# Performance work log

Measured on AMD Instinct MI355X. Metric: run time of the kernel, lower is better.

The kernel has to match this reference:

```python
import jax, jax.numpy as jnp
import numpy as np

NUM_HEAD = 8   # in_channels // 64 for in_channels=512
DIM = 8        # per-head dim (== num_head in this module)
H_CH = NUM_HEAD * DIM  # 64
SCALE = DIM ** (-0.5)


def _conv(x, w, b, padding):
    # x: [N,C,H,W], w: [O,I,kh,kw]
    out = jax.lax.conv_general_dilated(
        x, w, window_strides=(1, 1), padding=padding,
        dimension_numbers=("NCHW", "OIHW", "NCHW"))
    return out + b[None, :, None, None]


def setup_inputs() -> dict:
    key = jax.random.key(0)
    ks = jax.random.split(key, 4)
    N, C, H, W = 4, 512, 48, 48
    x = jax.random.normal(ks[0], (N, C, H, W), dtype=jnp.float32)
    qkv_w = jax.random.normal(ks[1], (3 * H_CH, C, 1, 1), dtype=jnp.float32) * 0.05
    qkv_b = jnp.zeros((3 * H_CH,), dtype=jnp.float32)
    pos_w = jax.random.normal(ks[2], (H_CH, H_CH, 3, 3), dtype=jnp.float32) * 0.05
    pos_b = jnp.zeros((H_CH,), dtype=jnp.float32)
    res_w = jax.random.normal(ks[3], (C, H_CH, 1, 1), dtype=jnp.float32) * 0.05
    res_b = jnp.zeros((C,), dtype=jnp.float32)
    return {"x": x, "qkv_w": qkv_w, "qkv_b": qkv_b,
            "pos_w": pos_w, "pos_b": pos_b,
            "res_w": res_w, "res_b": res_b}


def reference(x, qkv_w, qkv_b, pos_w, pos_b, res_w, res_b):
    N, C, H, W = x.shape
    L = H * W
    # 1x1 conv QKV projection -> [N, 3h, H, W]
    qkv = _conv(x, qkv_w, qkv_b, "VALID")
    # [N, num_head, 3*dim, L]
    qkv = qkv.reshape(N, NUM_HEAD, 3 * DIM, L)
    q, k, v = qkv[:, :, :DIM], qkv[:, :, DIM:2 * DIM], qkv[:, :, 2 * DIM:]
    # attn = q^T @ k * scale : [N, nh, L, L], softmax over keys (last dim)
    attn = jnp.einsum("nhdq,nhdk->nhqk", q, k) * SCALE
    attn = jax.nn.softmax(attn, axis=-1)
    # out = v @ attn^T : [N, nh, dim, L]
    out = jnp.einsum("nhdk,nhqk->nhdq", v, attn)
    out = out.reshape(N, H_CH, H, W)
    # positional branch: 3x3 conv on v
    pos = _conv(v.reshape(N, H_CH, H, W), pos_w, pos_b, "SAME")
    out = out + pos
    # resume 1x1 conv -> [N, out_channels, H, W]
    return _conv(out, res_w, res_b, "VALID")
```

## Files before the change

kernel.cpp:

```cpp
#include <hip/hip_runtime.h>

#define L_ATT 2304
#define QSCALE_LOG2E 0.5100695712f

using bh8 = __attribute__((ext_vector_type(8))) short;
using f4  = __attribute__((ext_vector_type(4))) float;

#if __has_builtin(__builtin_amdgcn_exp2f)
#define EXP2(x) __builtin_amdgcn_exp2f(x)
#else
#define EXP2(x) exp2f(x)
#endif

__device__ inline short f2b(float f) {
    union { float f; unsigned u; } c; c.f = f;
    unsigned r = (c.u + 0x7FFFu + ((c.u >> 16) & 1u)) >> 16;
    return (short)r;
}
__device__ inline float b2f(short s) {
    union { unsigned u; float f; } c;
    c.u = ((unsigned)(unsigned short)s) << 16;
    return c.f;
}
__device__ inline int packhi(float lo, float hi) {
    return (int)__builtin_amdgcn_perm(__float_as_uint(hi), __float_as_uint(lo), 0x07060302u);
}

__global__ __launch_bounds__(256) void prep_kernel(
    const float* __restrict__ x, const float* __restrict__ qkv_w,
    const float* __restrict__ res_w, const float* __restrict__ pos_w,
    short* __restrict__ xt, short* __restrict__ wqb,
    short* __restrict__ reswb, short* __restrict__ wqp)
{
    __shared__ float s[64][68];
    const int g = blockIdx.x;
    if (g < 272) {
        int j = g * 256 + threadIdx.x;
        if (j < 24576) {
            float4 v = ((const float4*)qkv_w)[j];
            short4 o = { f2b(v.x), f2b(v.y), f2b(v.z), f2b(v.w) };
            *(short4*)(wqb + (size_t)j * 4) = o;
        } else if (j < 32768) {
            int idx = j - 24576;
            float4 v = ((const float4*)res_w)[idx];
            short4 o = { f2b(v.x), f2b(v.y), f2b(v.z), f2b(v.w) };
            *(short4*)(reswb + (size_t)idx * 4) = o;
        } else {
            int e = j - 32768;
            wqp[e] = f2b(pos_w[(size_t)(e & 4095) * 9 + (e >> 12)]);
        }
        return;
    }
    const int gg = g - 272;
    const int l0 = (gg % 36) * 64, k0 = ((gg / 36) & 7) * 64, n = gg / 288;
    const int tr = threadIdx.x >> 4, tc4 = (threadIdx.x & 15) * 4;
    const float* xp = x + ((size_t)n * 512 + k0) * L_ATT + l0;
#pragma unroll
    for (int r = 0; r < 4; ++r)
        *(float4*)&s[tr + r * 16][tc4] =
            *(const float4*)(xp + (size_t)(tr + r * 16) * L_ATT + tc4);
    __syncthreads();
    short* op = xt + ((size_t)n * L_ATT + l0) * 512 + k0;
#pragma unroll
    for (int r = 0; r < 4; ++r) {
        int l = tr + r * 16;
        short4 o = { f2b(s[tc4 + 0][l]), f2b(s[tc4 + 1][l]),
                     f2b(s[tc4 + 2][l]), f2b(s[tc4 + 3][l]) };
        *(short4*)(op + (size_t)l * 512 + tc4) = o;
    }
}

__global__ __launch_bounds__(256) void qkv_kernel(
    const short* __restrict__ xt, const short* __restrict__ wqb,
    const float* __restrict__ qkv_b, short* __restrict__ qt8,
    short* __restrict__ kt8, short* __restrict__ vt, short* __restrict__ vle)
{
    const int g = blockIdx.x;
    const int xcd = g & 7, rr = g >> 3;
    const int y = rr % 3, grp = rr / 3;
    const int code = grp * 8 + xcd;
    const int l0 = (code % 72) * 32, oc0 = y * 64, n = code / 72;

    const int lane = threadIdx.x & 63, wave = threadIdx.x >> 6;
    const int col = lane & 15, quad = lane >> 4;
    const int ocb = oc0 + wave * 16;

    f4 acc[2];
    acc[0] = (f4){0.f, 0.f, 0.f, 0.f};
    acc[1] = (f4){0.f, 0.f, 0.f, 0.f};

    const short* arow = wqb + (size_t)(ocb + col) * 512 + quad * 8;
    const short* brow = xt + ((size_t)n * L_ATT + l0 + col) * 512 + quad * 8;

#pragma unroll 4
    for (int k0 = 0; k0 < 512; k0 += 32) {
        bh8 af = *(const bh8*)(arow + k0);
        bh8 b0 = *(const bh8*)(brow + k0);
        bh8 b1 = *(const bh8*)(brow + (size_t)16 * 512 + k0);
        acc[0] = __builtin_amdgcn_mfma_f32_16x16x32_bf16(af, b0, acc[0], 0, 0, 0);
        acc[1] = __builtin_amdgcn_mfma_f32_16x16x32_bf16(af, b1, acc[1], 0, 0, 0);
    }

    const int obase = ocb + quad * 4;
    const int h = obase / 24;
    const int r0 = obase - h * 24;
    const int slice = n * 8 + h;

#pragma unroll
    for (int nt = 0; nt < 2; ++nt) {
        int l = l0 + nt * 16 + col;
        float v[4];
#pragma unroll
        for (int reg = 0; reg < 4; ++reg) v[reg] = acc[nt][reg] + qkv_b[obase + reg];
        if (r0 < 8) {
            short4 o = { f2b(v[0] * QSCALE_LOG2E), f2b(v[1] * QSCALE_LOG2E),
                         f2b(v[2] * QSCALE_LOG2E), f2b(v[3] * QSCALE_LOG2E) };
            *(short4*)(qt8 + ((size_t)slice * L_ATT + l) * 8 + r0) = o;
        } else if (r0 < 16) {
            short4 o = { f2b(v[0]), f2b(v[1]), f2b(v[2]), f2b(v[3]) };
            *(short4*)(kt8 + ((size_t)slice * L_ATT + l) * 8 + (r0 - 8)) = o;
        } else {
            short4 o = { f2b(v[0]), f2b(v[1]), f2b(v[2]), f2b(v[3]) };
            int d0 = r0 - 16;
#pragma unroll
            for (int reg = 0; reg < 4; ++reg)
                vt[((size_t)slice * 8 + d0 + reg) * L_ATT + l] = ((short*)&o)[reg];
            *(short4*)(vle + ((size_t)n * L_ATT + l) * 64 + h * 8 + d0) = o;
        }
    }
}

__global__ __launch_bounds__(256) void attnpos_kernel(
    const short* __restrict__ qt8, const short* __restrict__ kt8,
    const short* __restrict__ vt, const short* __restrict__ vle,
    const short* __restrict__ wqp, const float* __restrict__ pbias,
    float* __restrict__ att, short* __restrict__ pcv)
{
    __shared__ short smem[2064];
    const int g = blockIdx.x;
    const int tid = threadIdx.x;
    const int lane = tid & 63, wave = tid >> 6;
    const int col = lane & 15, quad = lane >> 4;

    if (g < 576) {
        const int h = g & 7, r = g >> 3;
        const int n = r / 18, qt = r % 18;
        const int q0 = qt * 128;
        const int slice = n * 8 + h;

        const short* qs  = qt8 + (size_t)slice * L_ATT * 8;
        const short* ks8 = kt8 + (size_t)slice * L_ATT * 8;
        const short* vb  = vt  + (size_t)slice * 8 * L_ATT;

        if (tid < 16) smem[2048 + tid] = (tid < 8) ? (short)0x3F80 : (short)0;

        bh8 zero8 = {0, 0, 0, 0, 0, 0, 0, 0};
        bh8 qf[2];
#pragma unroll
        for (int f = 0; f < 2; ++f) {
            qf[f] = zero8;
            if (quad == 0)
                qf[f] = *(const bh8*)(qs + (size_t)(q0 + wave * 32 + f * 16 + col) * 8);
        }

        const int kxor = (quad == 0) ? 512 : 0;
        int kidx[4];
#pragma unroll
        for (int nt = 0; nt < 4; ++nt)
            kidx[nt] = (quad == 0) ? (nt * 16 + col) * 8 : 2056;
        const int vxor = (col < 8) ? 512 : 0;
        int vidx[2];
#pragma unroll
        for (int ks = 0; ks < 2; ++ks)
            vidx[ks] = (col < 8)
                     ? 1024 + col * 64 + ((ks * 32 + quad * 8 + col * 8) & 63)
                     : ((col == 8) ? 2048 : 2056);

        const int ksl = ((lane >> 5) & 1) * 32 + ((lane >> 2) & 1) * 16
                      + ((lane >> 3) & 3) * 4 + (lane & 3);
        const int vd = lane >> 3, vkc = (lane & 7) * 8;
        const int vsl = 1024 + vd * 64 + ((vkc + vd * 8) & 63);

        if (wave == 0)
            *(uint4*)&smem[ksl * 8] = *(const uint4*)(ks8 + (size_t)lane * 8);
        else if (wave == 1)
            *(uint4*)&smem[vsl] = *(const uint4*)(vb + (size_t)vd * L_ATT + vkc);
        __syncthreads();

        f4 oacc[2];
        oacc[0] = (f4){0.f, 0.f, 0.f, 0.f};
        oacc[1] = (f4){0.f, 0.f, 0.f, 0.f};

        int sofs = 512;
        for (int t = 0; t < 36; ++t) {
            uint4 dk, dv;
            if (wave == 0)
                dk = *(const uint4*)(ks8 + (size_t)((t + 1) * 64 + lane) * 8);
            else if (wave == 1)
                dv = *(const uint4*)(vb + (size_t)vd * L_ATT + (t + 1) * 64 + vkc);

            bh8 kf[4], vf[2];
#pragma unroll
            for (int nt = 0; nt < 4; ++nt) kf[nt] = *(const bh8*)&smem[kidx[nt]];
#pragma unroll
            for (int ks = 0; ks < 2; ++ks) vf[ks] = *(const bh8*)&smem[vidx[ks]];

#pragma unroll
            for (int f = 0; f < 2; ++f) {
                f4 s[4];
#pragma unroll
                for (int nt = 0; nt < 4; ++nt) {
                    f4 z = (f4){0.f, 0.f, 0.f, 0.f};
                    s[nt] = __builtin_amdgcn_mfma_f32_16x16x32_bf16(kf[nt], qf[f], z, 0, 0, 0);
                }
                float e[4][4];
#pragma unroll
                for (int nt = 0; nt < 4; ++nt)
#pragma unroll
                    for (int reg = 0; reg < 4; ++reg)
                        e[nt][reg] = EXP2(s[nt][reg]);
#pragma unroll
                for (int ks = 0; ks < 2; ++ks) {
                    union { int i[4]; bh8 v; } pu;
                    pu.i[0] = packhi(e[2 * ks][0],     e[2 * ks][1]);
                    pu.i[1] = packhi(e[2 * ks][2],     e[2 * ks][3]);
                    pu.i[2] = packhi(e[2 * ks + 1][0], e[2 * ks + 1][1]);
                    pu.i[3] = packhi(e[2 * ks + 1][2], e[2 * ks + 1][3]);
                    oacc[f] = __builtin_amdgcn_mfma_f32_16x16x32_bf16(vf[ks], pu.v, oacc[f], 0, 0, 0);
                }
            }

            if (wave == 0)      *(uint4*)&smem[sofs + ksl * 8] = dk;
            else if (wave == 1) *(uint4*)&smem[sofs + vsl] = dv;

#pragma unroll
            for (int nt = 0; nt < 4; ++nt) kidx[nt] ^= kxor;
            vidx[0] ^= vxor; vidx[1] ^= vxor;
            sofs ^= 512;
            __syncthreads();
        }

#pragma unroll
        for (int f = 0; f < 2; ++f) {
            float ls  = __shfl(oacc[f][0], 32 + col);
            float inv = 1.0f / ls;
            if (quad < 2) {
                int q = q0 + wave * 32 + f * 16 + col;
                float4 o = { oacc[f][0] * inv, oacc[f][1] * inv,
                             oacc[f][2] * inv, oacc[f][3] * inv };
                *(float4*)(att + ((size_t)n * L_ATT + q) * 64 + h * 8 + quad * 4) = o;
            }
        }
        return;
    }

    const int gf = g - 576;
    const int l0 = (gf % 144) * 16, n = gf / 144;
    const int t = wave;

    const int la = l0 + col;
    const int ya = la / 48, xa = la - ya * 48;

    f4 acc = (f4){0.f, 0.f, 0.f, 0.f};
    const short* vbase = vle + (size_t)n * L_ATT * 64;

#pragma unroll
    for (int q = 0; q < 9; ++q) {
        const int dy = q / 3 - 1, dx = q - (q / 3) * 3 - 1;
        const bool valid = ((unsigned)(ya + dy) < 48u) && ((unsigned)(xa + dx) < 48u);
        const short* ap = vbase + (size_t)(la + dy * 48 + dx) * 64 + quad * 8;
#pragma unroll
        for (int ks = 0; ks < 2; ++ks) {
            bh8 af = {0, 0, 0, 0, 0, 0, 0, 0};
            if (valid) af = *(const bh8*)(ap + ks * 32);
            bh8 bf = *(const bh8*)(wqp + ((size_t)q * 64 + t * 16 + col) * 64
                                   + ks * 32 + quad * 8);
            acc = __builtin_amdgcn_mfma_f32_16x16x32_bf16(af, bf, acc, 0, 0, 0);
        }
    }

    short* op = pcv + (size_t)n * L_ATT * 64;
    const int oc = t * 16 + col;
    const float bb = pbias[oc];
#pragma unroll
    for (int reg = 0; reg < 4; ++reg) {
        int l = l0 + quad * 4 + reg;
        op[(size_t)l * 64 + oc] = f2b(acc[reg] + bb);
    }
}

__global__ __launch_bounds__(256) void res_kernel(
    const float* __restrict__ att, const short* __restrict__ pcv,
    const short* __restrict__ reswb, const float* __restrict__ res_b,
    float* __restrict__ out)
{
    const int g = blockIdx.x;
    const int xcd = g & 7, rr = g >> 3;
    const int y = rr & 7, grp = rr >> 3;
    const int code = grp * 8 + xcd;
    const int l0 = (code % 36) * 64, oc0 = y * 64, n = code / 36;

    const int lane = threadIdx.x & 63, wave = threadIdx.x >> 6;
    const int col = lane & 15, quad = lane >> 4;
    const int ocb = oc0 + wave * 16;

    f4 acc[4];
#pragma unroll
    for (int nt = 0; nt < 4; ++nt) acc[nt] = (f4){0.f, 0.f, 0.f, 0.f};

#pragma unroll
    for (int ks = 0; ks < 2; ++ks) {
        bh8 af = *(const bh8*)(reswb + (size_t)(ocb + col) * 64 + ks * 32 + quad * 8);
        const int ch = ks * 32 + quad * 8;
#pragma unroll
        for (int nt = 0; nt < 4; ++nt) {
            const int l = l0 + nt * 16 + col;
            const float* ab = att + ((size_t)n * L_ATT + l) * 64 + ch;
            float4 a0 = *(const float4*)ab;
            float4 a1 = *(const float4*)(ab + 4);
            bh8 pv = *(const bh8*)(pcv + ((size_t)n * L_ATT + l) * 64 + ch);
            union { int i[4]; bh8 v; } pu;
            pu.i[0] = packhi(a0.x + b2f(pv[0]), a0.y + b2f(pv[1]));
            pu.i[1] = packhi(a0.z + b2f(pv[2]), a0.w + b2f(pv[3]));
            pu.i[2] = packhi(a1.x + b2f(pv[4]), a1.y + b2f(pv[5]));
            pu.i[3] = packhi(a1.z + b2f(pv[6]), a1.w + b2f(pv[7]));
            acc[nt] = __builtin_amdgcn_mfma_f32_16x16x32_bf16(af, pu.v, acc[nt], 0, 0, 0);
        }
    }

#pragma unroll
    for (int nt = 0; nt < 4; ++nt) {
        int l = l0 + nt * 16 + col;
#pragma unroll
        for (int reg = 0; reg < 4; ++reg) {
            int oc = ocb + quad * 4 + reg;
            out[((size_t)n * 512 + oc) * L_ATT + l] = acc[nt][reg] + res_b[oc];
        }
    }
}

extern "C" void kernel_launch(void* const* d_in, const int* in_sizes, int n_in,
                              void* d_out, int out_size, void* d_ws, size_t ws_size,
                              hipStream_t stream)
{
    const float* x      = (const float*)d_in[0];
    const float* qkv_w  = (const float*)d_in[1];
    const float* qkv_b  = (const float*)d_in[2];
    const float* pos_w  = (const float*)d_in[3];
    const float* pos_b  = (const float*)d_in[4];
    const float* res_w  = (const float*)d_in[5];
    const float* res_b  = (const float*)d_in[6];
    float* out = (float*)d_out;

    char* ws = (char*)d_ws;
    short* xt    = (short*)(ws);
    float* att   = (float*)(ws);
    short* qt8   = (short*)(ws + 9437184);
    short* kt8   = (short*)(ws + 10616832);
    short* vt    = (short*)(ws + 11796480);
    short* pcv   = (short*)(ws + 12976128);
    short* wqb   = (short*)(ws + 14155776);
    short* reswb = (short*)(ws + 14352384);
    short* vle   = (short*)(ws + 14417920);
    short* wqp   = (short*)(ws + 15597568);

    prep_kernel<<<1424, 256, 0, stream>>>(x, qkv_w, res_w, pos_w, xt, wqb, reswb, wqp);
    qkv_kernel<<<864, 256, 0, stream>>>(xt, wqb, qkv_b, qt8, kt8, vt, vle);
    attnpos_kernel<<<1152, 256, 0, stream>>>(qt8, kt8, vt, vle, wqp, pos_b, att, pcv);
    res_kernel<<<1152, 256, 0, stream>>>(att, pcv, reswb, res_b, out);
}
```

Baseline: 163.3 us.

## Halve attention query tile per block and double-step key/value staging

Attention blocks now cover 64 queries instead of 128, so the attention grid doubles from 576 to 1152 blocks and there are more waves to fill the GPU. Each wave keeps a single 16-query fragment instead of two. The K/V shared-memory ping-pong now stages two 64-key chunks per iteration, which halves the number of barriers per key pass. The cost is that K/V are reloaded from global memory twice as often across blocks, and shared memory per block doubles.

```diff
diff --git a/kernel.cpp b/kernel.cpp
--- a/kernel.cpp
+++ b/kernel.cpp
@@ -136,82 +136,81 @@
     const short* __restrict__ wqp, const float* __restrict__ pbias,
     float* __restrict__ att, short* __restrict__ pcv)
 {
-    __shared__ short smem[2064];
+    __shared__ short smem[4112];
     const int g = blockIdx.x;
     const int tid = threadIdx.x;
     const int lane = tid & 63, wave = tid >> 6;
     const int col = lane & 15, quad = lane >> 4;
 
-    if (g < 576) {
+    if (g < 1152) {
         const int h = g & 7, r = g >> 3;
-        const int n = r / 18, qt = r % 18;
-        const int q0 = qt * 128;
+        const int n = r / 36, qt = r % 36;
+        const int q0 = qt * 64;
         const int slice = n * 8 + h;
 
         const short* qs  = qt8 + (size_t)slice * L_ATT * 8;
         const short* ks8 = kt8 + (size_t)slice * L_ATT * 8;
         const short* vb  = vt  + (size_t)slice * 8 * L_ATT;
 
-        if (tid < 16) smem[2048 + tid] = (tid < 8) ? (short)0x3F80 : (short)0;
+        if (tid < 16) smem[4096 + tid] = (tid < 8) ? (short)0x3F80 : (short)0;
 
         bh8 zero8 = {0, 0, 0, 0, 0, 0, 0, 0};
-        bh8 qf[2];
-#pragma unroll
-        for (int f = 0; f < 2; ++f) {
-            qf[f] = zero8;
-            if (quad == 0)
-                qf[f] = *(const bh8*)(qs + (size_t)(q0 + wave * 32 + f * 16 + col) * 8);
-        }
-
-        const int kxor = (quad == 0) ? 512 : 0;
+        bh8 qf = zero8;
+        if (quad == 0)
+            qf = *(const bh8*)(qs + (size_t)(q0 + wave * 16 + col) * 8);
+
         int kidx[4];
 #pragma unroll
         for (int nt = 0; nt < 4; ++nt)
-            kidx[nt] = (quad == 0) ? (nt * 16 + col) * 8 : 2056;
-        const int vxor = (col < 8) ? 512 : 0;
+            kidx[nt] = (quad == 0) ? (nt * 16 + col) * 8 : 4104;
         int vidx[2];
 #pragma unroll
         for (int ks = 0; ks < 2; ++ks)
             vidx[ks] = (col < 8)
-                     ? 1024 + col * 64 + ((ks * 32 + quad * 8 + col * 8) & 63)
-                     : ((col == 8) ? 2048 : 2056);
+                     ? col * 64 + ((ks * 32 + quad * 8 + col * 8) & 63)
+                     : ((col == 8) ? 4096 : 4104);
 
         const int ksl = ((lane >> 5) & 1) * 32 + ((lane >> 2) & 1) * 16
                       + ((lane >> 3) & 3) * 4 + (lane & 3);
         const int vd = lane >> 3, vkc = (lane & 7) * 8;
-        const int vsl = 1024 + vd * 64 + ((vkc + vd * 8) & 63);
-
-        if (wave == 0)
-            *(uint4*)&smem[ksl * 8] = *(const uint4*)(ks8 + (size_t)lane * 8);
-        else if (wave == 1)
-            *(uint4*)&smem[vsl] = *(const uint4*)(vb + (size_t)vd * L_ATT + vkc);
+        const int vsl = vd * 64 + ((vkc + vd * 8) & 63);
+
+        if (wave == 0) {
+            *(uint4*)&smem[ksl * 8]       = *(const uint4*)(ks8 + (size_t)lane * 8);
+            *(uint4*)&smem[512 + ksl * 8] = *(const uint4*)(ks8 + (size_t)(64 + lane) * 8);
+        } else if (wave == 1) {
+            *(uint4*)&smem[2048 + vsl]       = *(const uint4*)(vb + (size_t)vd * L_ATT + vkc);
+            *(uint4*)&smem[2048 + 512 + vsl] = *(const uint4*)(vb + (size_t)vd * L_ATT + 64 + vkc);
+        }
         __syncthreads();
 
-        f4 oacc[2];
-        oacc[0] = (f4){0.f, 0.f, 0.f, 0.f};
-        oacc[1] = (f4){0.f, 0.f, 0.f, 0.f};
-
-        int sofs = 512;
-        for (int t = 0; t < 36; ++t) {
-            uint4 dk, dv;
-            if (wave == 0)
-                dk = *(const uint4*)(ks8 + (size_t)((t + 1) * 64 + lane) * 8);
-            else if (wave == 1)
-                dv = *(const uint4*)(vb + (size_t)vd * L_ATT + (t + 1) * 64 + vkc);
-
-            bh8 kf[4], vf[2];
-#pragma unroll
-            for (int nt = 0; nt < 4; ++nt) kf[nt] = *(const bh8*)&smem[kidx[nt]];
-#pragma unroll
-            for (int ks = 0; ks < 2; ++ks) vf[ks] = *(const bh8*)&smem[vidx[ks]];
-
-#pragma unroll
-            for (int f = 0; f < 2; ++f) {
+        f4 oacc = (f4){0.f, 0.f, 0.f, 0.f};
+        int p = 0;
+        for (int t = 0; t < 18; ++t) {
+            uint4 dk0, dk1, dv0, dv1;
+            if (wave == 0) {
+                dk0 = *(const uint4*)(ks8 + (size_t)((t * 2 + 2) * 64 + lane) * 8);
+                dk1 = *(const uint4*)(ks8 + (size_t)((t * 2 + 3) * 64 + lane) * 8);
+            } else if (wave == 1) {
+                dv0 = *(const uint4*)(vb + (size_t)vd * L_ATT + (t * 2 + 2) * 64 + vkc);
+                dv1 = *(const uint4*)(vb + (size_t)vd * L_ATT + (t * 2 + 3) * 64 + vkc);
+            }
+
+#pragma unroll
+            for (int u = 0; u < 2; ++u) {
+                const int ku = (quad == 0) ? p * 1024 + u * 512 : 0;
+                const int vu = (col < 8) ? 2048 + p * 1024 + u * 512 : 0;
+                bh8 kf[4], vf[2];
+#pragma unroll
+                for (int nt = 0; nt < 4; ++nt) kf[nt] = *(const bh8*)&smem[kidx[nt] + ku];
+#pragma unroll
+                for (int ks = 0; ks < 2; ++ks) vf[ks] = *(const bh8*)&smem[vidx[ks] + vu];
+
                 f4 s[4];
 #pragma unroll
                 for (int nt = 0; nt < 4; ++nt) {
                     f4 z = (f4){0.f, 0.f, 0.f, 0.f};
-                    s[nt] = __builtin_amdgcn_mfma_f32_16x16x32_bf16(kf[nt], qf[f], z, 0, 0, 0);
+                    s[nt] = __builtin_amdgcn_mfma_f32_16x16x32_bf16(kf[nt], qf, z, 0, 0, 0);
                 }
                 float e[4][4];
 #pragma unroll
@@ -226,35 +225,33 @@
                     pu.i[1] = packhi(e[2 * ks][2],     e[2 * ks][3]);
                     pu.i[2] = packhi(e[2 * ks + 1][0], e[2 * ks + 1][1]);
                     pu.i[3] = packhi(e[2 * ks + 1][2], e[2 * ks + 1][3]);
-                    oacc[f] = __builtin_amdgcn_mfma_f32_16x16x32_bf16(vf[ks], pu.v, oacc[f], 0, 0, 0);
+                    oacc = __builtin_amdgcn_mfma_f32_16x16x32_bf16(vf[ks], pu.v, oacc, 0, 0, 0);
                 }
             }
 
-            if (wave == 0)      *(uint4*)&smem[sofs + ksl * 8] = dk;
-            else if (wave == 1) *(uint4*)&smem[sofs + vsl] = dv;
-
-#pragma unroll
-            for (int nt = 0; nt < 4; ++nt) kidx[nt] ^= kxor;
-            vidx[0] ^= vxor; vidx[1] ^= vxor;
-            sofs ^= 512;
+            if (wave == 0) {
+                *(uint4*)&smem[(p ^ 1) * 1024 + ksl * 8]       = dk0;
+                *(uint4*)&smem[(p ^ 1) * 1024 + 512 + ksl * 8] = dk1;
+            } else if (wave == 1) {
+                *(uint4*)&smem[2048 + (p ^ 1) * 1024 + vsl]       = dv0;
+                *(uint4*)&smem[2048 + (p ^ 1) * 1024 + 512 + vsl] = dv1;
+            }
+            p ^= 1;
             __syncthreads();
         }
 
-#pragma unroll
-        for (int f = 0; f < 2; ++f) {
-            float ls  = __shfl(oacc[f][0], 32 + col);
-            float inv = 1.0f / ls;
-            if (quad < 2) {
-                int q = q0 + wave * 32 + f * 16 + col;
-                float4 o = { oacc[f][0] * inv, oacc[f][1] * inv,
-                             oacc[f][2] * inv, oacc[f][3] * inv };
-                *(float4*)(att + ((size_t)n * L_ATT + q) * 64 + h * 8 + quad * 4) = o;
-            }
+        float ls  = __shfl(oacc[0], 32 + col);
+        float inv = 1.0f / ls;
+        if (quad < 2) {
+            int q = q0 + wave * 16 + col;
+            float4 o = { oacc[0] * inv, oacc[1] * inv,
+                         oacc[2] * inv, oacc[3] * inv };
+            *(float4*)(att + ((size_t)n * L_ATT + q) * 64 + h * 8 + quad * 4) = o;
         }
         return;
     }
 
-    const int gf = g - 576;
+    const int gf = g - 1152;
     const int l0 = (gf % 144) * 16, n = gf / 144;
     const int t = wave;
 
@@ -366,6 +363,6 @@
 
     prep_kernel<<<1424, 256, 0, stream>>>(x, qkv_w, res_w, pos_w, xt, wqb, reswb, wqp);
     qkv_kernel<<<864, 256, 0, stream>>>(xt, wqb, qkv_b, qt8, kt8, vt, vle);
-    attnpos_kernel<<<1152, 256, 0, stream>>>(qt8, kt8, vt, vle, wqp, pos_b, att, pcv);
+    attnpos_kernel<<<1728, 256, 0, stream>>>(qt8, kt8, vt, vle, wqp, pos_b, att, pcv);
     res_kernel<<<1152, 256, 0, stream>>>(att, pcv, reswb, res_b, out);
 }
```

Result: faster. 156.6 us (-4.1%).
